# Kernel optimization log

Hardware: AMD Instinct MI355X
Metric: run time of the kernel (lower is better)

The kernel has to match this reference:

```python
import jax, jax.numpy as jnp
import numpy as np

D_MODEL = 1024
D_STATE = 16
D_CONV = 4
EXPAND = 2
D_INNER = D_MODEL * EXPAND          # 2048
DT_RANK = max(D_MODEL // 16, 1)     # 64
BATCH, SEQ_LEN = 2, 1024


def setup_inputs() -> dict:
    key = jax.random.key(0)
    ks = jax.random.split(key, 10)
    s = 0.02  # torch init std for linears
    x = jax.random.normal(ks[0], (BATCH, SEQ_LEN, D_MODEL), jnp.float32)
    W_in = jax.random.normal(ks[1], (2 * D_INNER, D_MODEL), jnp.float32) * s
    conv_w = jax.random.normal(ks[2], (D_INNER, 1, D_CONV), jnp.float32) * (1.0 / np.sqrt(D_CONV))
    conv_b = jnp.zeros((D_INNER,), jnp.float32)
    W_x = jax.random.normal(ks[3], (DT_RANK + 2 * D_STATE, D_INNER), jnp.float32) * s
    W_dt = jax.random.uniform(ks[4], (D_INNER, DT_RANK), jnp.float32,
                              -DT_RANK ** -0.5, DT_RANK ** -0.5)
    # dt bias init: inverse-softplus of dt ~ LogUniform(1e-3, 1e-1)
    dt = jnp.exp(jax.random.uniform(ks[5], (D_INNER,), jnp.float32)
                 * (np.log(0.1) - np.log(0.001)) + np.log(0.001))
    b_dt = dt + jnp.log(-jnp.expm1(-dt))
    A_log = jnp.log(jnp.tile(jnp.arange(1, D_STATE + 1, dtype=jnp.float32), (D_INNER, 1)))
    D_skip = jnp.ones((D_INNER,), jnp.float32)
    W_out = jax.random.normal(ks[6], (D_MODEL, D_INNER), jnp.float32) * s
    return {"x": x, "W_in": W_in, "conv_w": conv_w, "conv_b": conv_b, "W_x": W_x,
            "W_dt": W_dt, "b_dt": b_dt, "A_log": A_log, "D_skip": D_skip, "W_out": W_out}


def _causal_depthwise_conv(x_bld, conv_w, conv_b):
    # x_bld: [B, L, d_inner]; conv_w: [d_inner, 1, K]. Torch pads K-1 both
    # sides then slices [:seq_len] == causal left-pad of K-1.
    K = conv_w.shape[-1]
    lhs = jnp.pad(x_bld, ((0, 0), (K - 1, 0), (0, 0))).transpose(0, 2, 1)  # [B, C, L+K-1]
    out = jax.lax.conv_general_dilated(
        lhs, conv_w, window_strides=(1,), padding='VALID',
        dimension_numbers=('NCH', 'OIH', 'NCH'),
        feature_group_count=conv_w.shape[0])
    return out.transpose(0, 2, 1) + conv_b  # [B, L, d_inner]


def reference(x, W_in, conv_w, conv_b, W_x, W_dt, b_dt, A_log, D_skip, W_out):
    d_inner = W_in.shape[0] // 2
    dt_rank = W_dt.shape[1]
    d_state = A_log.shape[1]

    xz = jnp.einsum('bld,ed->ble', x, W_in)            # [B, L, 2*d_inner]
    x_ssm, z = xz[..., :d_inner], xz[..., d_inner:]
    x_ssm = jax.nn.silu(_causal_depthwise_conv(x_ssm, conv_w, conv_b))

    dbc = jnp.einsum('bld,ed->ble', x_ssm, W_x)        # [B, L, dt_rank+2*d_state]
    dt = jax.nn.softplus(jnp.einsum('blr,dr->bld', dbc[..., :dt_rank], W_dt) + b_dt)
    Bm = dbc[..., dt_rank:dt_rank + d_state]           # [B, L, d_state]
    Cm = dbc[..., dt_rank + d_state:]                  # [B, L, d_state]

    A = -jnp.exp(A_log)                                # [d_inner, d_state]
    A_bar = jnp.exp(dt[..., None] * A)                 # [B, L, d_inner, d_state]
    x_db = (x_ssm * dt)[..., None] * Bm[:, :, None, :] # [B, L, d_inner, d_state]

    def step(h, inp):
        a_t, xb_t, c_t = inp                           # [B,d,n], [B,d,n], [B,n]
        h = a_t * h + xb_t
        y_t = jnp.einsum('bn,bdn->bd', c_t, h)
        return h, y_t

    h0 = jnp.zeros((x.shape[0], d_inner, d_state), x.dtype)
    _, ys = jax.lax.scan(step, h0, (jnp.swapaxes(A_bar, 0, 1),
                                    jnp.swapaxes(x_db, 0, 1),
                                    jnp.swapaxes(Cm, 0, 1)))
    y = jnp.swapaxes(ys, 0, 1)                         # [B, L, d_inner]
    y = (y + x_ssm * D_skip) * jax.nn.silu(z)
    return jnp.einsum('bld,od->blo', y, W_out)         # [B, L, d_model]
```

## Files before the change

### kernel.cpp

```cpp
#include <hip/hip_runtime.h>
#include <hip/hip_bf16.h>
#include <math.h>

#define D_MODEL 1024
#define D_STATE 16
#define D_INNER 2048
#define DT_RANK 64
#define BATCH 2
#define SEQ_LEN 1024
#define T_TOTAL (BATCH * SEQ_LEN)

#define NC 64
#define CL 16

#define KS 16
#define KC 128
#define KT 64

typedef unsigned short u16;
typedef __bf16 bf16x8 __attribute__((ext_vector_type(8)));
typedef float f32x4 __attribute__((ext_vector_type(4)));

__device__ __forceinline__ u16 f2bf(float f) {
    unsigned u = __builtin_bit_cast(unsigned, f);
    u += 0x7FFFu + ((u >> 16) & 1u);
    return (u16)(u >> 16);
}

#define GLOAD_LDS16(g, l) \
    __builtin_amdgcn_global_load_lds((const __attribute__((address_space(1))) void*)(g), \
                                     (__attribute__((address_space(3))) void*)(l), 16, 0, 0)

__global__ __launch_bounds__(256) void cast3_bf16_kernel(
    const float* __restrict__ in0, u16* __restrict__ out0, int nb0,
    const float* __restrict__ in1, u16* __restrict__ out1, int nb1,
    const float* __restrict__ in2, u16* __restrict__ out2)
{
    const float* in; u16* out; int i;
    if (blockIdx.x < nb0) {
        in = in0; out = out0; i = blockIdx.x * 256 + threadIdx.x;
    } else if (blockIdx.x < nb0 + nb1) {
        in = in1; out = out1; i = (blockIdx.x - nb0) * 256 + threadIdx.x;
    } else {
        in = in2; out = out2; i = (blockIdx.x - nb0 - nb1) * 256 + threadIdx.x;
    }
    float4 v = ((const float4*)in)[i];
    unsigned lo = (unsigned)f2bf(v.x) | ((unsigned)f2bf(v.y) << 16);
    unsigned hi = (unsigned)f2bf(v.z) | ((unsigned)f2bf(v.w) << 16);
    ((uint2*)out)[i] = make_uint2(lo, hi);
}

__global__ __launch_bounds__(512) void gemm_bf16_8w(
    const u16* __restrict__ A, int lda,
    const u16* __restrict__ Bw, int ldb,
    float* __restrict__ C, int ldc, int kchunk, size_t csize)
{
    __shared__ u16 As[128][64];
    __shared__ u16 Bs[128][64];

    const int tid  = threadIdx.x;
    const int lane = tid & 63;
    const int wave = tid >> 6;
    const int wr   = wave >> 2;
    const int wc   = wave & 3;
    const int row0 = blockIdx.y * 128;
    const int col0 = blockIdx.x * 128;
    const int kbase = blockIdx.z * kchunk;

    C += (size_t)blockIdx.z * csize;

    const int srow = tid >> 3;
    const int scol = (tid & 7) * 8;

    const u16* ag = A  + (size_t)(row0 + srow) * lda + scol;
    const u16* bg = Bw + (size_t)(col0 + srow) * ldb + scol;
    u16* asl = &As[0][0] + wave * 512;
    u16* bsl = &Bs[0][0] + wave * 512;

    f32x4 acc[4][2];
#pragma unroll
    for (int m = 0; m < 4; ++m)
#pragma unroll
        for (int n = 0; n < 2; ++n)
            acc[m][n] = (f32x4){0.f, 0.f, 0.f, 0.f};

    const int fr = lane & 15;
    const int kh = (lane >> 4) * 8;

    for (int k0 = kbase; k0 < kbase + kchunk; k0 += 64) {
        GLOAD_LDS16(ag + k0,                     asl);
        GLOAD_LDS16(ag + k0 + (size_t)64 * lda,  asl + 4096);
        GLOAD_LDS16(bg + k0,                     bsl);
        GLOAD_LDS16(bg + k0 + (size_t)64 * ldb,  bsl + 4096);
        __syncthreads();

#pragma unroll
        for (int kk = 0; kk < 64; kk += 32) {
            bf16x8 af[4], bf[2];
#pragma unroll
            for (int m = 0; m < 4; ++m)
                af[m] = *(const bf16x8*)&As[wr * 64 + m * 16 + fr][kk + kh];
#pragma unroll
            for (int n = 0; n < 2; ++n)
                bf[n] = *(const bf16x8*)&Bs[wc * 32 + n * 16 + fr][kk + kh];
#pragma unroll
            for (int m = 0; m < 4; ++m)
#pragma unroll
                for (int n = 0; n < 2; ++n)
                    acc[m][n] = __builtin_amdgcn_mfma_f32_16x16x32_bf16(
                        af[m], bf[n], acc[m][n], 0, 0, 0);
        }
        __syncthreads();
    }

    const int crow = (lane >> 4) * 4;
#pragma unroll
    for (int m = 0; m < 4; ++m) {
        const int gr = row0 + wr * 64 + m * 16 + crow;
#pragma unroll
        for (int n = 0; n < 2; ++n) {
            const int gc = col0 + wc * 32 + n * 16 + fr;
#pragma unroll
            for (int r = 0; r < 4; ++r)
                C[(size_t)(gr + r) * ldc + gc] = acc[m][n][r];
        }
    }
}

__global__ __launch_bounds__(256) void reduce2_kernel(
    const float* __restrict__ part, float* __restrict__ out, size_t n4)
{
    size_t i = (size_t)blockIdx.x * 256 + threadIdx.x;
    float4 a = ((const float4*)part)[i];
    float4 b = ((const float4*)part)[i + n4];
    ((float4*)out)[i] = make_float4(a.x + b.x, a.y + b.y, a.z + b.z, a.w + b.w);
}

__global__ __launch_bounds__(256) void wx_partial(
    const float* __restrict__ A,
    const float* __restrict__ Bw,
    float* __restrict__ part)
{
    __shared__ float As[32][68];
    __shared__ float Bs[KT][98];

    const int tid = threadIdx.x;
    const int ks  = blockIdx.x;
    const int m0  = blockIdx.y * 32;
    const int k0  = ks * KC;

    const int tx = tid & 15;
    const int ty = tid >> 4;

    float acc[2][6] = {};

    for (int kk = 0; kk < KC; kk += KT) {
#pragma unroll
        for (int i = 0; i < 2; ++i) {
            int slot = tid + i * 256;
            int m  = slot >> 4;
            int kq = slot & 15;
            float4 v = *(const float4*)&A[(size_t)(m0 + m) * D_INNER + k0 + kk + kq * 4];
            *(float4*)&As[m][kq * 4] = v;
        }
#pragma unroll
        for (int i = 0; i < 6; ++i) {
            int slot = tid + i * 256;
            int n  = slot >> 4;
            int kq = slot & 15;
            float4 v = *(const float4*)&Bw[(size_t)n * D_INNER + k0 + kk + kq * 4];
            Bs[kq * 4 + 0][n] = v.x;
            Bs[kq * 4 + 1][n] = v.y;
            Bs[kq * 4 + 2][n] = v.z;
            Bs[kq * 4 + 3][n] = v.w;
        }
        __syncthreads();

#pragma unroll 8
        for (int k = 0; k < KT; ++k) {
            float a0 = As[ty * 2 + 0][k];
            float a1 = As[ty * 2 + 1][k];
            float2 b0 = *(const float2*)&Bs[k][tx * 6 + 0];
            float2 b1 = *(const float2*)&Bs[k][tx * 6 + 2];
            float2 b2 = *(const float2*)&Bs[k][tx * 6 + 4];
            float bv[6] = {b0.x, b0.y, b1.x, b1.y, b2.x, b2.y};
#pragma unroll
            for (int j = 0; j < 6; ++j) {
                acc[0][j] += a0 * bv[j];
                acc[1][j] += a1 * bv[j];
            }
        }
        __syncthreads();
    }

#pragma unroll
    for (int i = 0; i < 2; ++i) {
        size_t base = ((size_t)ks * T_TOTAL + (m0 + ty * 2 + i)) * 96 + tx * 6;
#pragma unroll
        for (int j = 0; j < 6; ++j)
            part[base + j] = acc[i][j];
    }
}

__global__ __launch_bounds__(256) void wx_reduce(
    const float* __restrict__ part, float* __restrict__ dbc)
{
    int i = blockIdx.x * 256 + threadIdx.x;
    float s = 0.f;
#pragma unroll
    for (int ks = 0; ks < KS; ++ks)
        s += part[(size_t)ks * T_TOTAL * 96 + i];
    dbc[i] = s;
}

__global__ __launch_bounds__(256) void dt_gemm(
    const float* __restrict__ A,
    const float* __restrict__ Bw,
    const float* __restrict__ bdt,
    float* __restrict__ dtb)
{
    __shared__ float As[16][65];
    __shared__ float Bs[16][65];

    const int tid = threadIdx.x;
    const int row0 = blockIdx.y * 64;
    const int col0 = blockIdx.x * 64;
    const int ty = tid >> 4;
    const int tx = tid & 15;

    float acc[4][4] = {};

    for (int k0 = 0; k0 < DT_RANK; k0 += 16) {
#pragma unroll
        for (int i = 0; i < 4; ++i) {
            int idx = tid + i * 256;
            int m = idx >> 4;
            int k = idx & 15;
            As[k][m] = A[(size_t)(row0 + m) * 96 + (k0 + k)];
        }
#pragma unroll
        for (int i = 0; i < 4; ++i) {
            int idx = tid + i * 256;
            int n = idx >> 4;
            int k = idx & 15;
            Bs[k][n] = Bw[(size_t)(col0 + n) * DT_RANK + (k0 + k)];
        }
        __syncthreads();

#pragma unroll
        for (int k = 0; k < 16; ++k) {
            float a[4], b[4];
#pragma unroll
            for (int i = 0; i < 4; ++i) a[i] = As[k][ty * 4 + i];
#pragma unroll
            for (int j = 0; j < 4; ++j) b[j] = Bs[k][tx * 4 + j];
#pragma unroll
            for (int i = 0; i < 4; ++i)
#pragma unroll
                for (int j = 0; j < 4; ++j)
                    acc[i][j] += a[i] * b[j];
        }
        __syncthreads();
    }

#pragma unroll
    for (int i = 0; i < 4; ++i) {
        int gm = row0 + ty * 4 + i;
#pragma unroll
        for (int j = 0; j < 4; ++j) {
            int gn = col0 + tx * 4 + j;
            float xv = acc[i][j] + bdt[gn];
            float sp = (xv > 20.f) ? xv : log1pf(__expf(xv));
            dtb[(size_t)gm * D_INNER + gn] = sp;
        }
    }
}

__global__ __launch_bounds__(256) void conv_silu_kernel(
    const float* __restrict__ xz,
    const float* __restrict__ cw,
    const float* __restrict__ cb,
    float* __restrict__ xc)
{
    int idx = blockIdx.x * 256 + threadIdx.x;
    int d = idx & (D_INNER - 1);
    int t = (idx >> 11) & (SEQ_LEN - 1);
    int b = idx >> 21;

    const float* base = xz + ((size_t)b * SEQ_LEN + t) * (2 * D_INNER) + d;
    float w0 = cw[d * 4 + 0], w1 = cw[d * 4 + 1], w2 = cw[d * 4 + 2], w3 = cw[d * 4 + 3];
    float acc = cb[d];
    if (t >= 3) acc += w0 * base[-3 * (2 * D_INNER)];
    if (t >= 2) acc += w1 * base[-2 * (2 * D_INNER)];
    if (t >= 1) acc += w2 * base[-1 * (2 * D_INNER)];
    acc += w3 * base[0];
    float s = acc / (1.f + __expf(-acc));
    xc[idx] = s;
}

__global__ __launch_bounds__(256) void scanA(
    const float* __restrict__ dbc,
    const float* __restrict__ dtv,
    const float* __restrict__ xc,
    const float* __restrict__ A_log,
    float* __restrict__ hbuf,
    float* __restrict__ sdt)
{
    __shared__ float sB[CL][16];

    const int tid = threadIdx.x;
    const int c = blockIdx.x;
    const int b = blockIdx.z;
    const int d = blockIdx.y * 256 + tid;
    const int t0 = c * CL;

    {
        int t = tid >> 4, e = tid & 15;
        sB[t][e] = dbc[(size_t)(b * SEQ_LEN + t0 + t) * 96 + DT_RANK + e];
    }

    float A[16];
#pragma unroll
    for (int i = 0; i < 4; ++i) {
        float4 v = *(const float4*)&A_log[d * 16 + i * 4];
        A[i * 4 + 0] = -__expf(v.x);
        A[i * 4 + 1] = -__expf(v.y);
        A[i * 4 + 2] = -__expf(v.z);
        A[i * 4 + 3] = -__expf(v.w);
    }
    __syncthreads();

    float h[16];
#pragma unroll
    for (int n = 0; n < 16; ++n) h[n] = 0.f;
    float sum = 0.f;

#pragma unroll 4
    for (int t = 0; t < CL; ++t) {
        size_t row = (size_t)(b * SEQ_LEN + t0 + t);
        float dtval = dtv[row * D_INNER + d];
        float xv    = xc [row * D_INNER + d];
        float w = xv * dtval;
        sum += dtval;
#pragma unroll
        for (int n = 0; n < 16; ++n) {
            float a = __expf(dtval * A[n]);
            h[n] = a * h[n] + w * sB[t][n];
        }
    }

    size_t o = (size_t)(b * NC + c) * 16 * D_INNER + d;
#pragma unroll
    for (int n = 0; n < 16; ++n)
        hbuf[o + (size_t)n * D_INNER] = h[n];
    sdt[(size_t)(b * NC + c) * D_INNER + d] = sum;
}

__global__ __launch_bounds__(256) void scanB(
    const float* __restrict__ A_log,
    const float* __restrict__ sdt,
    float* __restrict__ hbuf)
{
    int idx = blockIdx.x * 256 + threadIdx.x;
    int b  = idx >> 15;
    int nd = idx & 32767;
    int n  = nd >> 11;
    int d  = nd & (D_INNER - 1);

    const float A = -__expf(A_log[d * 16 + n]);
    float h = 0.f;
#pragma unroll 8
    for (int c = 0; c < NC; ++c) {
        size_t o = ((size_t)(b * NC + c) * 16 + n) * D_INNER + d;
        float tmp = hbuf[o];
        float P = __expf(A * sdt[(size_t)(b * NC + c) * D_INNER + d]);
        hbuf[o] = h;
        h = P * h + tmp;
    }
}

__global__ __launch_bounds__(256) void scanC(
    const float* __restrict__ dbc,
    const float* __restrict__ dtv,
    const float* __restrict__ xc,
    const float* __restrict__ xz,
    const float* __restrict__ A_log,
    const float* __restrict__ D_skip,
    const float* __restrict__ hbuf,
    u16* __restrict__ y)
{
    __shared__ float sB[CL][16];
    __shared__ float sC[CL][16];

    const int tid = threadIdx.x;
    const int c = blockIdx.x;
    const int b = blockIdx.z;
    const int d = blockIdx.y * 256 + tid;
    const int t0 = c * CL;

    {
        int t = tid >> 4, e = tid & 15;
        size_t row = (size_t)(b * SEQ_LEN + t0 + t);
        sB[t][e] = dbc[row * 96 + DT_RANK + e];
        sC[t][e] = dbc[row * 96 + DT_RANK + D_STATE + e];
    }

    float A[16];
#pragma unroll
    for (int i = 0; i < 4; ++i) {
        float4 v = *(const float4*)&A_log[d * 16 + i * 4];
        A[i * 4 + 0] = -__expf(v.x);
        A[i * 4 + 1] = -__expf(v.y);
        A[i * 4 + 2] = -__expf(v.z);
        A[i * 4 + 3] = -__expf(v.w);
    }
    const float Dv = D_skip[d];

    float h[16];
    size_t ho = (size_t)(b * NC + c) * 16 * D_INNER + d;
#pragma unroll
    for (int n = 0; n < 16; ++n)
        h[n] = hbuf[ho + (size_t)n * D_INNER];
    __syncthreads();

#pragma unroll 4
    for (int t = 0; t < CL; ++t) {
        size_t row = (size_t)(b * SEQ_LEN + t0 + t);
        float dtval = dtv[row * D_INNER + d];
        float xv    = xc [row * D_INNER + d];
        float zv    = xz [row * (2 * D_INNER) + D_INNER + d];
        float w = xv * dtval;
        float yv = 0.f;
#pragma unroll
        for (int n = 0; n < 16; ++n) {
            float a = __expf(dtval * A[n]);
            h[n] = a * h[n] + w * sB[t][n];
            yv += sC[t][n] * h[n];
        }
        float sig = 1.f / (1.f + __expf(-zv));
        y[row * D_INNER + d] = f2bf((yv + xv * Dv) * (zv * sig));
    }
}

extern "C" void kernel_launch(void* const* d_in, const int* in_sizes, int n_in,
                              void* d_out, int out_size, void* d_ws, size_t ws_size,
                              hipStream_t stream)
{
    const float* x      = (const float*)d_in[0];
    const float* W_in   = (const float*)d_in[1];
    const float* conv_w = (const float*)d_in[2];
    const float* conv_b = (const float*)d_in[3];
    const float* W_x    = (const float*)d_in[4];
    const float* W_dt   = (const float*)d_in[5];
    const float* b_dt   = (const float*)d_in[6];
    const float* A_log  = (const float*)d_in[7];
    const float* D_skip = (const float*)d_in[8];
    const float* W_out  = (const float*)d_in[9];
    float* out = (float*)d_out;

    float* ws = (float*)d_ws;
    float* xz    = ws;
    float* xc    = xz + (size_t)8388608;
    float* dbc   = xc + (size_t)4194304;
    float* dtbuf = dbc + (size_t)196608;
    float* hbuf  = dtbuf + (size_t)4194304;
    float* sdt   = hbuf + (size_t)4194304;
    u16* ybf = (u16*)(sdt + (size_t)262144);
    u16* xbf = ybf + (size_t)4194304;
    u16* wbf = xbf + (size_t)2097152;
    u16* wobf = wbf + (size_t)4194304;
    float* part = dtbuf;
    float* part7 = hbuf;

    cast3_bf16_kernel<<<8192, 256, 0, stream>>>(x, xbf, 2048,
                                                W_in, wbf, 4096,
                                                W_out, wobf);

    {
        dim3 grid(4096 / 128, 2048 / 128, 1);
        gemm_bf16_8w<<<grid, 512, 0, stream>>>(xbf, D_MODEL, wbf, D_MODEL,
                                               xz, 2 * D_INNER, D_MODEL, 0);
    }
    conv_silu_kernel<<<(T_TOTAL * D_INNER) / 256, 256, 0, stream>>>(xz, conv_w, conv_b, xc);

    {
        dim3 grid(KS, T_TOTAL / 32);
        wx_partial<<<grid, 256, 0, stream>>>(xc, W_x, part);
        wx_reduce<<<(T_TOTAL * 96) / 256, 256, 0, stream>>>(part, dbc);
    }
    {
        dim3 grid(D_INNER / 64, T_TOTAL / 64);
        dt_gemm<<<grid, 256, 0, stream>>>(dbc, W_dt, b_dt, dtbuf);
    }
    {
        dim3 gridA(NC, D_INNER / 256, BATCH);
        scanA<<<gridA, 256, 0, stream>>>(dbc, dtbuf, xc, A_log, hbuf, sdt);
        scanB<<<(BATCH * D_STATE * D_INNER) / 256, 256, 0, stream>>>(A_log, sdt, hbuf);
        scanC<<<gridA, 256, 0, stream>>>(dbc, dtbuf, xc, xz,
                                         A_log, D_skip, hbuf, ybf);
    }
    {
        dim3 grid(1024 / 128, 2048 / 128, 2);
        gemm_bf16_8w<<<grid, 512, 0, stream>>>(ybf, D_INNER, wobf, D_INNER,
                                               part7, D_MODEL, 1024,
                                               (size_t)T_TOTAL * D_MODEL);
        reduce2_kernel<<<(T_TOTAL * D_MODEL / 4) / 256, 256, 0, stream>>>(
            part7, out, (size_t)T_TOTAL * D_MODEL / 4);
    }
}
```

Before: 271.8 us.

## Fuse middle Mamba stages into one cooperative persistent kernel with grid syncs

Replaces the seven middle launches (conv+silu, W_x partial GEMM and reduce, dt GEMM, three scan phases) with a single cooperative kernel that loops over work units and separates phases with grid-wide syncs. The aim is to remove per-kernel launch gaps and tail effects between small dependent stages. In exchange, the grid is capped at the occupancy-limited resident block count, so wide phases like conv and the scans run with fewer concurrent blocks. Grid.sync also carries its own cost, and the host now queries device attributes and occupancy on every launch. The old multi-kernel path is kept as a fallback.

```diff
diff --git a/kernel.cpp b/kernel.cpp
--- a/kernel.cpp
+++ b/kernel.cpp
@@ -1,6 +1,9 @@
 #include <hip/hip_runtime.h>
 #include <hip/hip_bf16.h>
+#include <hip/hip_cooperative_groups.h>
 #include <math.h>
+
+namespace cg = cooperative_groups;
 
 #define D_MODEL 1024
 #define D_STATE 16
@@ -136,24 +139,37 @@
     ((float4*)out)[i] = make_float4(a.x + b.x, a.y + b.y, a.z + b.z, a.w + b.w);
 }
 
+__global__ __launch_bounds__(256) void conv_silu_kernel(
+    const float* __restrict__ xz, const float* __restrict__ cw,
+    const float* __restrict__ cb, float* __restrict__ xc)
+{
+    int idx = blockIdx.x * 256 + threadIdx.x;
+    int d = idx & (D_INNER - 1);
+    int t = (idx >> 11) & (SEQ_LEN - 1);
+    int b = idx >> 21;
+    const float* base = xz + ((size_t)b * SEQ_LEN + t) * (2 * D_INNER) + d;
+    float w0 = cw[d * 4 + 0], w1 = cw[d * 4 + 1], w2 = cw[d * 4 + 2], w3 = cw[d * 4 + 3];
+    float acc = cb[d];
+    if (t >= 3) acc += w0 * base[-3 * (2 * D_INNER)];
+    if (t >= 2) acc += w1 * base[-2 * (2 * D_INNER)];
+    if (t >= 1) acc += w2 * base[-1 * (2 * D_INNER)];
+    acc += w3 * base[0];
+    xc[idx] = acc / (1.f + __expf(-acc));
+}
+
 __global__ __launch_bounds__(256) void wx_partial(
-    const float* __restrict__ A,
-    const float* __restrict__ Bw,
+    const float* __restrict__ A, const float* __restrict__ Bw,
     float* __restrict__ part)
 {
     __shared__ float As[32][68];
     __shared__ float Bs[KT][98];
-
     const int tid = threadIdx.x;
     const int ks  = blockIdx.x;
     const int m0  = blockIdx.y * 32;
     const int k0  = ks * KC;
-
     const int tx = tid & 15;
     const int ty = tid >> 4;
-
     float acc[2][6] = {};
-
     for (int kk = 0; kk < KC; kk += KT) {
 #pragma unroll
         for (int i = 0; i < 2; ++i) {
@@ -175,7 +191,6 @@
             Bs[kq * 4 + 3][n] = v.w;
         }
         __syncthreads();
-
 #pragma unroll 8
         for (int k = 0; k < KT; ++k) {
             float a0 = As[ty * 2 + 0][k];
@@ -192,7 +207,6 @@
         }
         __syncthreads();
     }
-
 #pragma unroll
     for (int i = 0; i < 2; ++i) {
         size_t base = ((size_t)ks * T_TOTAL + (m0 + ty * 2 + i)) * 96 + tx * 6;
@@ -214,22 +228,17 @@
 }
 
 __global__ __launch_bounds__(256) void dt_gemm(
-    const float* __restrict__ A,
-    const float* __restrict__ Bw,
-    const float* __restrict__ bdt,
-    float* __restrict__ dtb)
+    const float* __restrict__ A, const float* __restrict__ Bw,
+    const float* __restrict__ bdt, float* __restrict__ dtb)
 {
     __shared__ float As[16][65];
     __shared__ float Bs[16][65];
-
     const int tid = threadIdx.x;
     const int row0 = blockIdx.y * 64;
     const int col0 = blockIdx.x * 64;
     const int ty = tid >> 4;
     const int tx = tid & 15;
-
     float acc[4][4] = {};
-
     for (int k0 = 0; k0 < DT_RANK; k0 += 16) {
 #pragma unroll
         for (int i = 0; i < 4; ++i) {
@@ -246,7 +255,6 @@
             Bs[k][n] = Bw[(size_t)(col0 + n) * DT_RANK + (k0 + k)];
         }
         __syncthreads();
-
 #pragma unroll
         for (int k = 0; k < 16; ++k) {
             float a[4], b[4];
@@ -262,7 +270,6 @@
         }
         __syncthreads();
     }
-
 #pragma unroll
     for (int i = 0; i < 4; ++i) {
         int gm = row0 + ty * 4 + i;
@@ -276,49 +283,21 @@
     }
 }
 
-__global__ __launch_bounds__(256) void conv_silu_kernel(
-    const float* __restrict__ xz,
-    const float* __restrict__ cw,
-    const float* __restrict__ cb,
-    float* __restrict__ xc)
-{
-    int idx = blockIdx.x * 256 + threadIdx.x;
-    int d = idx & (D_INNER - 1);
-    int t = (idx >> 11) & (SEQ_LEN - 1);
-    int b = idx >> 21;
-
-    const float* base = xz + ((size_t)b * SEQ_LEN + t) * (2 * D_INNER) + d;
-    float w0 = cw[d * 4 + 0], w1 = cw[d * 4 + 1], w2 = cw[d * 4 + 2], w3 = cw[d * 4 + 3];
-    float acc = cb[d];
-    if (t >= 3) acc += w0 * base[-3 * (2 * D_INNER)];
-    if (t >= 2) acc += w1 * base[-2 * (2 * D_INNER)];
-    if (t >= 1) acc += w2 * base[-1 * (2 * D_INNER)];
-    acc += w3 * base[0];
-    float s = acc / (1.f + __expf(-acc));
-    xc[idx] = s;
-}
-
 __global__ __launch_bounds__(256) void scanA(
-    const float* __restrict__ dbc,
-    const float* __restrict__ dtv,
-    const float* __restrict__ xc,
-    const float* __restrict__ A_log,
-    float* __restrict__ hbuf,
-    float* __restrict__ sdt)
+    const float* __restrict__ dbc, const float* __restrict__ dtv,
+    const float* __restrict__ xc, const float* __restrict__ A_log,
+    float* __restrict__ hbuf, float* __restrict__ sdt)
 {
     __shared__ float sB[CL][16];
-
     const int tid = threadIdx.x;
     const int c = blockIdx.x;
     const int b = blockIdx.z;
     const int d = blockIdx.y * 256 + tid;
     const int t0 = c * CL;
-
     {
         int t = tid >> 4, e = tid & 15;
         sB[t][e] = dbc[(size_t)(b * SEQ_LEN + t0 + t) * 96 + DT_RANK + e];
     }
-
     float A[16];
 #pragma unroll
     for (int i = 0; i < 4; ++i) {
@@ -329,12 +308,10 @@
         A[i * 4 + 3] = -__expf(v.w);
     }
     __syncthreads();
-
     float h[16];
 #pragma unroll
     for (int n = 0; n < 16; ++n) h[n] = 0.f;
     float sum = 0.f;
-
 #pragma unroll 4
     for (int t = 0; t < CL; ++t) {
         size_t row = (size_t)(b * SEQ_LEN + t0 + t);
@@ -348,7 +325,6 @@
             h[n] = a * h[n] + w * sB[t][n];
         }
     }
-
     size_t o = (size_t)(b * NC + c) * 16 * D_INNER + d;
 #pragma unroll
     for (int n = 0; n < 16; ++n)
@@ -357,8 +333,7 @@
 }
 
 __global__ __launch_bounds__(256) void scanB(
-    const float* __restrict__ A_log,
-    const float* __restrict__ sdt,
+    const float* __restrict__ A_log, const float* __restrict__ sdt,
     float* __restrict__ hbuf)
 {
     int idx = blockIdx.x * 256 + threadIdx.x;
@@ -366,7 +341,6 @@
     int nd = idx & 32767;
     int n  = nd >> 11;
     int d  = nd & (D_INNER - 1);
-
     const float A = -__expf(A_log[d * 16 + n]);
     float h = 0.f;
 #pragma unroll 8
@@ -380,31 +354,24 @@
 }
 
 __global__ __launch_bounds__(256) void scanC(
-    const float* __restrict__ dbc,
-    const float* __restrict__ dtv,
-    const float* __restrict__ xc,
-    const float* __restrict__ xz,
-    const float* __restrict__ A_log,
-    const float* __restrict__ D_skip,
-    const float* __restrict__ hbuf,
-    u16* __restrict__ y)
+    const float* __restrict__ dbc, const float* __restrict__ dtv,
+    const float* __restrict__ xc, const float* __restrict__ xz,
+    const float* __restrict__ A_log, const float* __restrict__ D_skip,
+    const float* __restrict__ hbuf, u16* __restrict__ y)
 {
     __shared__ float sB[CL][16];
     __shared__ float sC[CL][16];
-
     const int tid = threadIdx.x;
     const int c = blockIdx.x;
     const int b = blockIdx.z;
     const int d = blockIdx.y * 256 + tid;
     const int t0 = c * CL;
-
     {
         int t = tid >> 4, e = tid & 15;
         size_t row = (size_t)(b * SEQ_LEN + t0 + t);
         sB[t][e] = dbc[row * 96 + DT_RANK + e];
         sC[t][e] = dbc[row * 96 + DT_RANK + D_STATE + e];
     }
-
     float A[16];
 #pragma unroll
     for (int i = 0; i < 4; ++i) {
@@ -415,14 +382,12 @@
         A[i * 4 + 3] = -__expf(v.w);
     }
     const float Dv = D_skip[d];
-
     float h[16];
     size_t ho = (size_t)(b * NC + c) * 16 * D_INNER + d;
 #pragma unroll
     for (int n = 0; n < 16; ++n)
         h[n] = hbuf[ho + (size_t)n * D_INNER];
     __syncthreads();
-
 #pragma unroll 4
     for (int t = 0; t < CL; ++t) {
         size_t row = (size_t)(b * SEQ_LEN + t0 + t);
@@ -439,6 +404,280 @@
         }
         float sig = 1.f / (1.f + __expf(-zv));
         y[row * D_INNER + d] = f2bf((yv + xv * Dv) * (zv * sig));
+    }
+}
+
+__global__ __launch_bounds__(256, 2) void mamba_mid(
+    const float* __restrict__ xz, float* __restrict__ xc,
+    const float* __restrict__ cw, const float* __restrict__ cb,
+    const float* __restrict__ Wx, float* __restrict__ part,
+    float* __restrict__ dbc,
+    const float* __restrict__ Wdt, const float* __restrict__ bdt,
+    float* __restrict__ dtb,
+    const float* __restrict__ A_log, const float* __restrict__ D_skip,
+    float* __restrict__ hbuf, float* __restrict__ sdt_,
+    u16* __restrict__ y)
+{
+    cg::grid_group grid = cg::this_grid();
+    __shared__ __align__(16) char smem[33792];
+
+    const int tid = threadIdx.x;
+    const int bid = blockIdx.x;
+    const int nwg = gridDim.x;
+
+    for (int idx = bid * 256 + tid; idx < T_TOTAL * D_INNER; idx += nwg * 256) {
+        int d = idx & (D_INNER - 1);
+        int t = (idx >> 11) & (SEQ_LEN - 1);
+        int b = idx >> 21;
+        const float* base = xz + ((size_t)b * SEQ_LEN + t) * (2 * D_INNER) + d;
+        float w0 = cw[d * 4 + 0], w1 = cw[d * 4 + 1],
+              w2 = cw[d * 4 + 2], w3 = cw[d * 4 + 3];
+        float acc = cb[d];
+        if (t >= 3) acc += w0 * base[-3 * (2 * D_INNER)];
+        if (t >= 2) acc += w1 * base[-2 * (2 * D_INNER)];
+        if (t >= 1) acc += w2 * base[-1 * (2 * D_INNER)];
+        acc += w3 * base[0];
+        xc[idx] = acc / (1.f + __expf(-acc));
+    }
+    grid.sync();
+
+    {
+        float (*As)[68] = (float(*)[68])smem;
+        float (*Bs)[98] = (float(*)[98])(smem + 8704);
+        const int tx = tid & 15;
+        const int ty = tid >> 4;
+        for (int unit = bid; unit < 1024; unit += nwg) {
+            const int ks = unit & 15;
+            const int m0 = (unit >> 4) * 32;
+            const int k0 = ks * KC;
+            float acc[2][6] = {};
+            for (int kk = 0; kk < KC; kk += KT) {
+#pragma unroll
+                for (int i = 0; i < 2; ++i) {
+                    int slot = tid + i * 256;
+                    int m  = slot >> 4;
+                    int kq = slot & 15;
+                    float4 v = *(const float4*)&xc[(size_t)(m0 + m) * D_INNER + k0 + kk + kq * 4];
+                    *(float4*)&As[m][kq * 4] = v;
+                }
+#pragma unroll
+                for (int i = 0; i < 6; ++i) {
+                    int slot = tid + i * 256;
+                    int n  = slot >> 4;
+                    int kq = slot & 15;
+                    float4 v = *(const float4*)&Wx[(size_t)n * D_INNER + k0 + kk + kq * 4];
+                    Bs[kq * 4 + 0][n] = v.x;
+                    Bs[kq * 4 + 1][n] = v.y;
+                    Bs[kq * 4 + 2][n] = v.z;
+                    Bs[kq * 4 + 3][n] = v.w;
+                }
+                __syncthreads();
+#pragma unroll 8
+                for (int k = 0; k < KT; ++k) {
+                    float a0 = As[ty * 2 + 0][k];
+                    float a1 = As[ty * 2 + 1][k];
+                    float2 b0 = *(const float2*)&Bs[k][tx * 6 + 0];
+                    float2 b1 = *(const float2*)&Bs[k][tx * 6 + 2];
+                    float2 b2 = *(const float2*)&Bs[k][tx * 6 + 4];
+                    float bv[6] = {b0.x, b0.y, b1.x, b1.y, b2.x, b2.y};
+#pragma unroll
+                    for (int j = 0; j < 6; ++j) {
+                        acc[0][j] += a0 * bv[j];
+                        acc[1][j] += a1 * bv[j];
+                    }
+                }
+                __syncthreads();
+            }
+#pragma unroll
+            for (int i = 0; i < 2; ++i) {
+                size_t base = ((size_t)ks * T_TOTAL + (m0 + ty * 2 + i)) * 96 + tx * 6;
+#pragma unroll
+                for (int j = 0; j < 6; ++j)
+                    part[base + j] = acc[i][j];
+            }
+        }
+    }
+    grid.sync();
+
+    for (int i = bid * 256 + tid; i < T_TOTAL * 96; i += nwg * 256) {
+        float s = 0.f;
+#pragma unroll
+        for (int ks = 0; ks < KS; ++ks)
+            s += part[(size_t)ks * T_TOTAL * 96 + i];
+        dbc[i] = s;
+    }
+    grid.sync();
+
+    {
+        float (*As)[65] = (float(*)[65])smem;
+        float (*Bs)[65] = (float(*)[65])(smem + 4160);
+        const int ty = tid >> 4;
+        const int tx = tid & 15;
+        for (int unit = bid; unit < 1024; unit += nwg) {
+            const int row0 = (unit >> 5) * 64;
+            const int col0 = (unit & 31) * 64;
+            float acc[4][4] = {};
+            for (int k0 = 0; k0 < DT_RANK; k0 += 16) {
+#pragma unroll
+                for (int i = 0; i < 4; ++i) {
+                    int idx = tid + i * 256;
+                    int m = idx >> 4;
+                    int k = idx & 15;
+                    As[k][m] = dbc[(size_t)(row0 + m) * 96 + (k0 + k)];
+                }
+#pragma unroll
+                for (int i = 0; i < 4; ++i) {
+                    int idx = tid + i * 256;
+                    int n = idx >> 4;
+                    int k = idx & 15;
+                    Bs[k][n] = Wdt[(size_t)(col0 + n) * DT_RANK + (k0 + k)];
+                }
+                __syncthreads();
+#pragma unroll
+                for (int k = 0; k < 16; ++k) {
+                    float a[4], b[4];
+#pragma unroll
+                    for (int i = 0; i < 4; ++i) a[i] = As[k][ty * 4 + i];
+#pragma unroll
+                    for (int j = 0; j < 4; ++j) b[j] = Bs[k][tx * 4 + j];
+#pragma unroll
+                    for (int i = 0; i < 4; ++i)
+#pragma unroll
+                        for (int j = 0; j < 4; ++j)
+                            acc[i][j] += a[i] * b[j];
+                }
+                __syncthreads();
+            }
+#pragma unroll
+            for (int i = 0; i < 4; ++i) {
+                int gm = row0 + ty * 4 + i;
+#pragma unroll
+                for (int j = 0; j < 4; ++j) {
+                    int gn = col0 + tx * 4 + j;
+                    float xv = acc[i][j] + bdt[gn];
+                    float sp = (xv > 20.f) ? xv : log1pf(__expf(xv));
+                    dtb[(size_t)gm * D_INNER + gn] = sp;
+                }
+            }
+        }
+    }
+    grid.sync();
+
+    {
+        float (*sB)[16] = (float(*)[16])smem;
+        for (int unit = bid; unit < 1024; unit += nwg) {
+            const int c = unit & 63;
+            const int b = unit >> 9;
+            const int d = ((unit >> 6) & 7) * 256 + tid;
+            const int t0 = c * CL;
+            {
+                int t = tid >> 4, e = tid & 15;
+                sB[t][e] = dbc[(size_t)(b * SEQ_LEN + t0 + t) * 96 + DT_RANK + e];
+            }
+            float A[16];
+#pragma unroll
+            for (int i = 0; i < 4; ++i) {
+                float4 v = *(const float4*)&A_log[d * 16 + i * 4];
+                A[i * 4 + 0] = -__expf(v.x);
+                A[i * 4 + 1] = -__expf(v.y);
+                A[i * 4 + 2] = -__expf(v.z);
+                A[i * 4 + 3] = -__expf(v.w);
+            }
+            __syncthreads();
+            float h[16];
+#pragma unroll
+            for (int n = 0; n < 16; ++n) h[n] = 0.f;
+            float sum = 0.f;
+#pragma unroll 4
+            for (int t = 0; t < CL; ++t) {
+                size_t row = (size_t)(b * SEQ_LEN + t0 + t);
+                float dtval = dtb[row * D_INNER + d];
+                float xv    = xc [row * D_INNER + d];
+                float w = xv * dtval;
+                sum += dtval;
+#pragma unroll
+                for (int n = 0; n < 16; ++n) {
+                    float a = __expf(dtval * A[n]);
+                    h[n] = a * h[n] + w * sB[t][n];
+                }
+            }
+            size_t o = (size_t)(b * NC + c) * 16 * D_INNER + d;
+#pragma unroll
+            for (int n = 0; n < 16; ++n)
+                hbuf[o + (size_t)n * D_INNER] = h[n];
+            sdt_[(size_t)(b * NC + c) * D_INNER + d] = sum;
+            __syncthreads();
+        }
+    }
+    grid.sync();
+
+    for (int idx = bid * 256 + tid; idx < BATCH * D_STATE * D_INNER; idx += nwg * 256) {
+        int b  = idx >> 15;
+        int nd = idx & 32767;
+        int n  = nd >> 11;
+        int d  = nd & (D_INNER - 1);
+        const float A = -__expf(A_log[d * 16 + n]);
+        float h = 0.f;
+#pragma unroll 8
+        for (int c = 0; c < NC; ++c) {
+            size_t o = ((size_t)(b * NC + c) * 16 + n) * D_INNER + d;
+            float tmp = hbuf[o];
+            float P = __expf(A * sdt_[(size_t)(b * NC + c) * D_INNER + d]);
+            hbuf[o] = h;
+            h = P * h + tmp;
+        }
+    }
+    grid.sync();
+
+    {
+        float (*sB)[16] = (float(*)[16])smem;
+        float (*sC)[16] = (float(*)[16])(smem + CL * 16 * 4);
+        for (int unit = bid; unit < 1024; unit += nwg) {
+            const int c = unit & 63;
+            const int b = unit >> 9;
+            const int d = ((unit >> 6) & 7) * 256 + tid;
+            const int t0 = c * CL;
+            {
+                int t = tid >> 4, e = tid & 15;
+                size_t row = (size_t)(b * SEQ_LEN + t0 + t);
+                sB[t][e] = dbc[row * 96 + DT_RANK + e];
+                sC[t][e] = dbc[row * 96 + DT_RANK + D_STATE + e];
+            }
+            float A[16];
+#pragma unroll
+            for (int i = 0; i < 4; ++i) {
+                float4 v = *(const float4*)&A_log[d * 16 + i * 4];
+                A[i * 4 + 0] = -__expf(v.x);
+                A[i * 4 + 1] = -__expf(v.y);
+                A[i * 4 + 2] = -__expf(v.z);
+                A[i * 4 + 3] = -__expf(v.w);
+            }
+            const float Dv = D_skip[d];
+            float h[16];
+            size_t ho = (size_t)(b * NC + c) * 16 * D_INNER + d;
+#pragma unroll
+            for (int n = 0; n < 16; ++n)
+                h[n] = hbuf[ho + (size_t)n * D_INNER];
+            __syncthreads();
+#pragma unroll 4
+            for (int t = 0; t < CL; ++t) {
+                size_t row = (size_t)(b * SEQ_LEN + t0 + t);
+                float dtval = dtb[row * D_INNER + d];
+                float xv    = xc [row * D_INNER + d];
+                float zv    = xz [row * (2 * D_INNER) + D_INNER + d];
+                float w = xv * dtval;
+                float yv = 0.f;
+#pragma unroll
+                for (int n = 0; n < 16; ++n) {
+                    float a = __expf(dtval * A[n]);
+                    h[n] = a * h[n] + w * sB[t][n];
+                    yv += sC[t][n] * h[n];
+                }
+                float sig = 1.f / (1.f + __expf(-zv));
+                y[row * D_INNER + d] = f2bf((yv + xv * Dv) * (zv * sig));
+            }
+            __syncthreads();
+        }
     }
 }
 
@@ -481,24 +720,44 @@
         gemm_bf16_8w<<<grid, 512, 0, stream>>>(xbf, D_MODEL, wbf, D_MODEL,
                                                xz, 2 * D_INNER, D_MODEL, 0);
     }
-    conv_silu_kernel<<<(T_TOTAL * D_INNER) / 256, 256, 0, stream>>>(xz, conv_w, conv_b, xc);
-
-    {
-        dim3 grid(KS, T_TOTAL / 32);
-        wx_partial<<<grid, 256, 0, stream>>>(xc, W_x, part);
-        wx_reduce<<<(T_TOTAL * 96) / 256, 256, 0, stream>>>(part, dbc);
-    }
-    {
-        dim3 grid(D_INNER / 64, T_TOTAL / 64);
-        dt_gemm<<<grid, 256, 0, stream>>>(dbc, W_dt, b_dt, dtbuf);
-    }
-    {
-        dim3 gridA(NC, D_INNER / 256, BATCH);
-        scanA<<<gridA, 256, 0, stream>>>(dbc, dtbuf, xc, A_log, hbuf, sdt);
-        scanB<<<(BATCH * D_STATE * D_INNER) / 256, 256, 0, stream>>>(A_log, sdt, hbuf);
-        scanC<<<gridA, 256, 0, stream>>>(dbc, dtbuf, xc, xz,
-                                         A_log, D_skip, hbuf, ybf);
-    }
+
+    int nCU = 0, maxB = 0, dev = 0;
+    (void)hipGetDevice(&dev);
+    (void)hipDeviceGetAttribute(&nCU, hipDeviceAttributeMultiprocessorCount, dev);
+    (void)hipOccupancyMaxActiveBlocksPerMultiprocessor(&maxB, mamba_mid, 256, 0);
+    int coop_grid = maxB * nCU;
+    if (coop_grid > 1024) coop_grid = 1024;
+
+    if (coop_grid >= 256) {
+        void* kargs[] = {
+            (void*)&xz, (void*)&xc, (void*)&conv_w, (void*)&conv_b,
+            (void*)&W_x, (void*)&part, (void*)&dbc,
+            (void*)&W_dt, (void*)&b_dt, (void*)&dtbuf,
+            (void*)&A_log, (void*)&D_skip,
+            (void*)&hbuf, (void*)&sdt, (void*)&ybf
+        };
+        (void)hipLaunchCooperativeKernel((void*)mamba_mid, dim3(coop_grid),
+                                         dim3(256), kargs, 0, stream);
+    } else {
+        conv_silu_kernel<<<(T_TOTAL * D_INNER) / 256, 256, 0, stream>>>(xz, conv_w, conv_b, xc);
+        {
+            dim3 grid(KS, T_TOTAL / 32);
+            wx_partial<<<grid, 256, 0, stream>>>(xc, W_x, part);
+            wx_reduce<<<(T_TOTAL * 96) / 256, 256, 0, stream>>>(part, dbc);
+        }
+        {
+            dim3 grid(D_INNER / 64, T_TOTAL / 64);
+            dt_gemm<<<grid, 256, 0, stream>>>(dbc, W_dt, b_dt, dtbuf);
+        }
+        {
+            dim3 gridA(NC, D_INNER / 256, BATCH);
+            scanA<<<gridA, 256, 0, stream>>>(dbc, dtbuf, xc, A_log, hbuf, sdt);
+            scanB<<<(BATCH * D_STATE * D_INNER) / 256, 256, 0, stream>>>(A_log, sdt, hbuf);
+            scanC<<<gridA, 256, 0, stream>>>(dbc, dtbuf, xc, xz,
+                                             A_log, D_skip, hbuf, ybf);
+        }
+    }
+
     {
         dim3 grid(1024 / 128, 2048 / 128, 2);
         gemm_bf16_8w<<<grid, 512, 0, stream>>>(ybf, D_INNER, wobf, D_INNER,
```

Result: slower. 581.6 us (+113.9%).
